# Performance work log

Hardware: AMD Instinct MI355X
Metric: run time of the kernel (lower is better)

The kernel has to match this reference:

```python
import jax, jax.numpy as jnp
import numpy as np

N_NODES = 100000
N_EDGES = 1200000
N_GRAPHS = 1000
HID = 64
OUT = 4
ALPHA_FLAG = 0.03
NEG_SLOPE = 0.2


def _glorot(key, shape):
    fan_in, fan_out = shape[0], shape[-1]
    lim = (6.0 / (fan_in + fan_out)) ** 0.5
    return jax.random.uniform(key, shape, jnp.float32, -lim, lim)


def setup_inputs() -> dict:
    key = jax.random.key(0)
    ks = jax.random.split(key, 32)
    inp = {
        "x": jax.random.normal(ks[0], (N_NODES, 8), jnp.float32),
        "edge_index": jax.random.randint(ks[1], (2, N_EDGES), 0, N_NODES, jnp.int32),
        "batch": jnp.sort(jax.random.randint(ks[2], (N_NODES,), 0, N_GRAPHS, jnp.int32)),
        "climber": jax.random.normal(ks[3], (N_GRAPHS, 6), jnp.float32),
        # lin_in
        "W_in": _glorot(ks[4], (6, HID)), "b_in": jnp.zeros((HID,), jnp.float32),
        # climber_embed: LayerNorm(6) + Linear(6,64)
        "ln_g": jnp.ones((6,), jnp.float32), "ln_b": jnp.zeros((6,), jnp.float32),
        "W_c": _glorot(ks[5], (6, HID)), "b_c": jnp.zeros((HID,), jnp.float32),
        # film1 / film2: Linear(64,128)
        "Wf1": _glorot(ks[6], (HID, 2 * HID)), "bf1": jnp.zeros((2 * HID,), jnp.float32),
        "Wf2": _glorot(ks[7], (HID, 2 * HID)), "bf2": jnp.zeros((2 * HID,), jnp.float32),
        # GATConv 1 (heads=1): lin weight, att_src, att_dst, bias
        "Wg1": _glorot(ks[8], (HID, HID)), "as1": _glorot(ks[9], (HID, 1))[:, 0],
        "ad1": _glorot(ks[10], (HID, 1))[:, 0], "bg1": jnp.zeros((HID,), jnp.float32),
        # GATConv 2
        "Wg2": _glorot(ks[11], (HID, HID)), "as2": _glorot(ks[12], (HID, 1))[:, 0],
        "ad2": _glorot(ks[13], (HID, 1))[:, 0], "bg2": jnp.zeros((HID,), jnp.float32),
        # cls head
        "Wc1": _glorot(ks[14], (HID, HID)), "bc1": jnp.zeros((HID,), jnp.float32),
        "Wc2": _glorot(ks[15], (HID, OUT)), "bc2": jnp.zeros((OUT,), jnp.float32),
        # flag head
        "Wh1": _glorot(ks[16], (2, 8)), "bh1": jnp.zeros((8,), jnp.float32),
        "Wh2": _glorot(ks[17], (8, OUT)), "bh2": jnp.zeros((OUT,), jnp.float32),
    }
    return inp


def _gat(h, src, dst, W, a_src, a_dst, bias, n):
    # PyG GATConv, heads=1, concat=False, self-loops already appended.
    z = h @ W                                    # [N, H]
    e = jax.nn.leaky_relu((z @ a_src)[src] + (z @ a_dst)[dst], NEG_SLOPE)  # [E]
    m = jax.ops.segment_max(e, dst, num_segments=n)
    ex = jnp.exp(e - m[dst])
    s = jax.ops.segment_sum(ex, dst, num_segments=n)
    alpha = ex / (s[dst] + 1e-16)
    out = jax.ops.segment_sum(alpha[:, None] * z[src], dst, num_segments=n)
    return out + bias


def reference(x, edge_index, batch, climber, W_in, b_in, ln_g, ln_b, W_c, b_c,
              Wf1, bf1, Wf2, bf2, Wg1, as1, ad1, bg1, Wg2, as2, ad2, bg2,
              Wc1, bc1, Wc2, bc2, Wh1, bh1, Wh2, bh2):
    n = x.shape[0]
    # add self loops (PyG GATConv default)
    loop = jnp.arange(n, dtype=edge_index.dtype)
    src = jnp.concatenate([edge_index[0], loop])
    dst = jnp.concatenate([edge_index[1], loop])

    x_cont, flags = x[:, :6], x[:, 6:8]
    h = x_cont @ W_in + b_in

    # climber embed: LayerNorm + Linear + ReLU
    mu = jnp.mean(climber, -1, keepdims=True)
    var = jnp.var(climber, -1, keepdims=True)
    cn = (climber - mu) * jax.lax.rsqrt(var + 1e-5) * ln_g + ln_b
    c = jax.nn.relu(cn @ W_c + b_c)

    def film(h, Wf, bf):
        gb = c @ Wf + bf
        gamma, beta = jnp.split(gb, 2, axis=-1)
        return h * (1.0 + gamma[batch]) + beta[batch]

    h = film(h, Wf1, bf1)
    h = jax.nn.relu(_gat(h, src, dst, Wg1, as1, ad1, bg1, n))
    h = film(h, Wf2, bf2)
    h = jax.nn.relu(_gat(h, src, dst, Wg2, as2, ad2, bg2, n))

    # cls head (dropout inactive in eval)
    cls = jax.nn.relu(h @ Wc1 + bc1) @ Wc2 + bc2
    flag = jax.nn.relu(flags @ Wh1 + bh1) @ Wh2 + bh2
    return cls + ALPHA_FLAG * flag
```

## Files before the change

### kernel.cpp

```cpp
#include <hip/hip_runtime.h>
#include <math.h>

#define N_NODES 100000
#define N_EDGES 1200000
#define N_GRAPHS 1000
#define HID 64
#define NBUCK 256
#define NPB   391
#define BCAP  8192
#define EDGE_CHUNK 16384
#define S3_BLOCKS ((N_EDGES + EDGE_CHUNK - 1) / EDGE_CHUNK)
#define LOG2E 1.4426950408889634f
#define N_TILES (N_NODES / 16)
#define MFMA_BLOCKS 391

typedef _Float16 half_t;
typedef __attribute__((ext_vector_type(4))) _Float16 half4;
typedef __attribute__((ext_vector_type(8))) _Float16 half8;
typedef __attribute__((ext_vector_type(4))) float floatx4;

__global__ void k_climber_film(const float* __restrict__ climber,
                               const float* __restrict__ ln_g, const float* __restrict__ ln_b,
                               const float* __restrict__ W_c, const float* __restrict__ b_c,
                               const float* __restrict__ Wf1, const float* __restrict__ bf1,
                               const float* __restrict__ Wf2, const float* __restrict__ bf2,
                               float* __restrict__ gb1, float* __restrict__ gb2,
                               int* __restrict__ bucket_fill) {
    __shared__ float cl[64];
    int g = blockIdx.x;
    int j = threadIdx.x;
    if (g == 0) {
        bucket_fill[j] = 0;
        bucket_fill[j + 128] = 0;
    }
    if (j < 64) {
        float v[6];
        float mu = 0.f;
        #pragma unroll
        for (int k = 0; k < 6; k++) { v[k] = climber[g*6+k]; mu += v[k]; }
        mu *= (1.f/6.f);
        float var = 0.f;
        #pragma unroll
        for (int k = 0; k < 6; k++) { float d = v[k]-mu; var += d*d; }
        var *= (1.f/6.f);
        float rs = rsqrtf(var + 1e-5f);
        float acc = b_c[j];
        #pragma unroll
        for (int k = 0; k < 6; k++) {
            float cn = (v[k]-mu)*rs*ln_g[k] + ln_b[k];
            acc += cn * W_c[k*64+j];
        }
        cl[j] = fmaxf(acc, 0.f);
    }
    __syncthreads();
    float a1 = bf1[j], a2 = bf2[j];
    #pragma unroll 8
    for (int k = 0; k < 64; k++) {
        float ck = cl[k];
        a1 += ck * Wf1[k*128+j];
        a2 += ck * Wf2[k*128+j];
    }
    gb1[g*128+j] = a1;
    gb2[g*128+j] = a2;
}


__global__ void k_bin(const int* __restrict__ ei, int* __restrict__ bucket_fill,
                      int* __restrict__ staged) {
    __shared__ int hist[NBUCK];
    __shared__ int cursor[NBUCK];
    for (int t = threadIdx.x; t < NBUCK; t += blockDim.x) hist[t] = 0;
    __syncthreads();
    int e0 = blockIdx.x * EDGE_CHUNK;
    int e1 = min(e0 + EDGE_CHUNK, N_EDGES);
    for (int e = e0 + threadIdx.x; e < e1; e += blockDim.x)
        atomicAdd(&hist[ei[N_EDGES + e] / NPB], 1);
    __syncthreads();
    if (threadIdx.x < NBUCK) {
        int hv = hist[threadIdx.x];
        int start = threadIdx.x * BCAP;
        if (hv) start += atomicAdd(&bucket_fill[threadIdx.x], hv);
        cursor[threadIdx.x] = start;
    }
    __syncthreads();
    for (int e = e0 + threadIdx.x; e < e1; e += blockDim.x) {
        int src = ei[e], dst = ei[N_EDGES + e];
        int b = dst / NPB;
        int ldst = dst - b * NPB;
        int pos = atomicAdd(&cursor[b], 1);
        staged[pos] = (ldst << 17) | src;
    }
}

__global__ void k_bcsr(const int* __restrict__ staged, const int* __restrict__ bucket_fill,
                       int* __restrict__ rowptr, int* __restrict__ csr_src) {
    __shared__ int bb[NBUCK];
    __shared__ int ldeg[NPB];
    __shared__ int sc[512];
    __shared__ int cursor[NPB];
    int b = blockIdx.x;
    if (threadIdx.x < NBUCK) bb[threadIdx.x] = bucket_fill[threadIdx.x];
    __syncthreads();
    for (int off = 1; off < NBUCK; off <<= 1) {
        int u = 0;
        if (threadIdx.x < NBUCK && threadIdx.x >= off) u = bb[threadIdx.x - off];
        __syncthreads();
        if (threadIdx.x < NBUCK) bb[threadIdx.x] += u;
        __syncthreads();
    }
    int bbase = (b == 0) ? 0 : bb[b-1];
    int bcnt  = bb[b] - bbase;
    const int* st = staged + b * BCAP;
    int n0 = b * NPB;
    int n1 = min(n0 + NPB, N_NODES);
    int nn = n1 - n0;
    for (int t = threadIdx.x; t < NPB; t += blockDim.x) ldeg[t] = 0;
    __syncthreads();
    for (int k = threadIdx.x; k < bcnt; k += blockDim.x)
        atomicAdd(&ldeg[st[k] >> 17], 1);
    __syncthreads();
    if (threadIdx.x < 512) sc[threadIdx.x] = (threadIdx.x < nn) ? ldeg[threadIdx.x] : 0;
    __syncthreads();
    for (int off = 1; off < 512; off <<= 1) {
        int u = 0;
        if (threadIdx.x < 512 && threadIdx.x >= off) u = sc[threadIdx.x - off];
        __syncthreads();
        if (threadIdx.x < 512) sc[threadIdx.x] += u;
        __syncthreads();
    }
    if (threadIdx.x < nn) {
        int pre = sc[threadIdx.x] - ldeg[threadIdx.x];
        rowptr[n0 + threadIdx.x] = bbase + pre;
        cursor[threadIdx.x] = bbase + pre;
    }
    if (b == 0 && threadIdx.x == 0) rowptr[N_NODES] = bb[NBUCK-1];
    __syncthreads();
    for (int k = threadIdx.x; k < bcnt; k += blockDim.x) {
        int v = st[k];
        int pos = atomicAdd(&cursor[v >> 17], 1);
        csr_src[pos] = v & 0x1FFFF;
    }
}

__global__ __launch_bounds__(256) void k_mfma_z1(
        const float* __restrict__ x, const int* __restrict__ batch,
        const float* __restrict__ W_in, const float* __restrict__ b_in,
        const float* __restrict__ gb1, const float* __restrict__ W,
        const float* __restrict__ a_src, const float* __restrict__ a_dst,
        half_t* __restrict__ z, float* __restrict__ es, float* __restrict__ ed) {
    __shared__ float Wi[384];
    __shared__ float bi[64];
    __shared__ half_t zl[4][16*64];
    for (int idx = threadIdx.x; idx < 384; idx += 256) Wi[idx] = W_in[idx];
    if (threadIdx.x < 64) bi[threadIdx.x] = b_in[threadIdx.x];
    int wave = threadIdx.x >> 6;
    int l    = threadIdx.x & 63;
    int c    = l & 15;
    int g    = l >> 4;
    half8 Bf[2][4];
    #pragma unroll
    for (int ko = 0; ko < 2; ko++) {
        #pragma unroll
        for (int nt = 0; nt < 4; nt++) {
            half8 bvec;
            #pragma unroll
            for (int j = 0; j < 8; j++)
                bvec[j] = (half_t)W[(ko*32 + g*8 + j)*64 + c + 16*nt];
            Bf[ko][nt] = bvec;
        }
    }
    float as4[4], ad4[4];
    #pragma unroll
    for (int nt = 0; nt < 4; nt++) {
        as4[nt] = a_src[c + 16*nt] * LOG2E;
        ad4[nt] = a_dst[c + 16*nt] * LOG2E;
    }
    __syncthreads();
    int nWaves = gridDim.x * 4;
    int wid = blockIdx.x * 4 + wave;
    half_t* zw = zl[wave];
    for (int t = wid; t < N_TILES; t += nWaves) {
        int m0 = t * 16;
        int i = m0 + c;
        float xv[6];
        #pragma unroll
        for (int kk = 0; kk < 6; kk++) xv[kk] = x[i*8 + kk];
        int bg_ = batch[i];
        half8 A[2];
        #pragma unroll
        for (int s = 0; s < 2; s++) {
            int bk = s*32 + g*8;
            float acc[8];
            #pragma unroll
            for (int j = 0; j < 8; j++) acc[j] = bi[bk + j];
            #pragma unroll
            for (int kk = 0; kk < 6; kk++) {
                float xk = xv[kk];
                float4 w0 = *(const float4*)&Wi[kk*64 + bk];
                float4 w1 = *(const float4*)&Wi[kk*64 + bk + 4];
                acc[0] += xk*w0.x; acc[1] += xk*w0.y;
                acc[2] += xk*w0.z; acc[3] += xk*w0.w;
                acc[4] += xk*w1.x; acc[5] += xk*w1.y;
                acc[6] += xk*w1.z; acc[7] += xk*w1.w;
            }
            const float4* gbv = (const float4*)(gb1 + bg_*128);
            float4 ga0 = gbv[bk/4],      ga1 = gbv[bk/4 + 1];
            float4 be0 = gbv[16 + bk/4], be1 = gbv[16 + bk/4 + 1];
            half8 hv;
            hv[0] = (half_t)(acc[0]*(1.f+ga0.x) + be0.x);
            hv[1] = (half_t)(acc[1]*(1.f+ga0.y) + be0.y);
            hv[2] = (half_t)(acc[2]*(1.f+ga0.z) + be0.z);
            hv[3] = (half_t)(acc[3]*(1.f+ga0.w) + be0.w);
            hv[4] = (half_t)(acc[4]*(1.f+ga1.x) + be1.x);
            hv[5] = (half_t)(acc[5]*(1.f+ga1.y) + be1.y);
            hv[6] = (half_t)(acc[6]*(1.f+ga1.z) + be1.z);
            hv[7] = (half_t)(acc[7]*(1.f+ga1.w) + be1.w);
            A[s] = hv;
        }
        floatx4 D[4];
        #pragma unroll
        for (int nt = 0; nt < 4; nt++) {
            floatx4 acc = {0.f, 0.f, 0.f, 0.f};
            acc = __builtin_amdgcn_mfma_f32_16x16x32_f16(A[0], Bf[0][nt], acc, 0, 0, 0);
            acc = __builtin_amdgcn_mfma_f32_16x16x32_f16(A[1], Bf[1][nt], acc, 0, 0, 0);
            D[nt] = acc;
        }
        #pragma unroll
        for (int r = 0; r < 4; r++) {
            float ps = D[0][r]*as4[0] + D[1][r]*as4[1] + D[2][r]*as4[2] + D[3][r]*as4[3];
            float pd = D[0][r]*ad4[0] + D[1][r]*ad4[1] + D[2][r]*ad4[2] + D[3][r]*ad4[3];
            #pragma unroll
            for (int off = 1; off < 16; off <<= 1) {
                ps += __shfl_xor(ps, off, 16);
                pd += __shfl_xor(pd, off, 16);
            }
            if (c == 0) {
                es[m0 + g*4 + r] = ps;
                ed[m0 + g*4 + r] = pd;
            }
        }
        #pragma unroll
        for (int nt = 0; nt < 4; nt++) {
            #pragma unroll
            for (int r = 0; r < 4; r++)
                zw[(g*4 + r)*64 + c + 16*nt] = (half_t)D[nt][r];
        }
        __asm__ __volatile__("s_waitcnt lgkmcnt(0)" ::: "memory");
        const half8* zr = (const half8*)zw;
        half8 v0 = zr[l*2];
        half8 v1 = zr[l*2 + 1];
        half8* zo = (half8*)(z + (size_t)m0 * 64);
        zo[l*2]     = v0;
        zo[l*2 + 1] = v1;
        __asm__ __volatile__("s_waitcnt lgkmcnt(0)" ::: "memory");
    }
}

__global__ __launch_bounds__(256) void k_mfma_z(
        const half_t* __restrict__ h, const float* __restrict__ W,
        const float* __restrict__ a_src, const float* __restrict__ a_dst,
        half_t* __restrict__ z, float* __restrict__ es, float* __restrict__ ed) {
    __shared__ half_t zl[4][16*64];
    int wave = threadIdx.x >> 6;
    int l    = threadIdx.x & 63;
    int c    = l & 15;
    int g    = l >> 4;
    half8 Bf[2][4];
    #pragma unroll
    for (int ko = 0; ko < 2; ko++) {
        #pragma unroll
        for (int nt = 0; nt < 4; nt++) {
            half8 b;
            #pragma unroll
            for (int j = 0; j < 8; j++)
                b[j] = (half_t)W[(ko*32 + g*8 + j)*64 + c + 16*nt];
            Bf[ko][nt] = b;
        }
    }
    float as4[4], ad4[4];
    #pragma unroll
    for (int nt = 0; nt < 4; nt++) {
        as4[nt] = a_src[c + 16*nt] * LOG2E;
        ad4[nt] = a_dst[c + 16*nt] * LOG2E;
    }
    int nWaves = gridDim.x * 4;
    int wid = blockIdx.x * 4 + wave;
    half_t* zw = zl[wave];
    for (int t = wid; t < N_TILES; t += nWaves) {
        int m0 = t * 16;
        const half8* hrow = (const half8*)(h + (size_t)(m0 + c) * 64);
        half8 A0 = hrow[g];
        half8 A1 = hrow[g + 4];
        floatx4 D[4];
        #pragma unroll
        for (int nt = 0; nt < 4; nt++) {
            floatx4 acc = {0.f, 0.f, 0.f, 0.f};
            acc = __builtin_amdgcn_mfma_f32_16x16x32_f16(A0, Bf[0][nt], acc, 0, 0, 0);
            acc = __builtin_amdgcn_mfma_f32_16x16x32_f16(A1, Bf[1][nt], acc, 0, 0, 0);
            D[nt] = acc;
        }
        #pragma unroll
        for (int r = 0; r < 4; r++) {
            float ps = D[0][r]*as4[0] + D[1][r]*as4[1] + D[2][r]*as4[2] + D[3][r]*as4[3];
            float pd = D[0][r]*ad4[0] + D[1][r]*ad4[1] + D[2][r]*ad4[2] + D[3][r]*ad4[3];
            #pragma unroll
            for (int off = 1; off < 16; off <<= 1) {
                ps += __shfl_xor(ps, off, 16);
                pd += __shfl_xor(pd, off, 16);
            }
            if (c == 0) {
                es[m0 + g*4 + r] = ps;
                ed[m0 + g*4 + r] = pd;
            }
        }
        #pragma unroll
        for (int nt = 0; nt < 4; nt++) {
            #pragma unroll
            for (int r = 0; r < 4; r++)
                zw[(g*4 + r)*64 + c + 16*nt] = (half_t)D[nt][r];
        }
        __asm__ __volatile__("s_waitcnt lgkmcnt(0)" ::: "memory");
        const half8* zr = (const half8*)zw;
        half8 v0 = zr[l*2];
        half8 v1 = zr[l*2 + 1];
        half8* zo = (half8*)(z + (size_t)m0 * 64);
        zo[l*2]     = v0;
        zo[l*2 + 1] = v1;
        __asm__ __volatile__("s_waitcnt lgkmcnt(0)" ::: "memory");
    }
}

__device__ __forceinline__ float4 h4_to_f4(half4 h) {
    float4 f;
    f.x = (float)h.x; f.y = (float)h.y; f.z = (float)h.z; f.w = (float)h.w;
    return f;
}

__global__ void k_agg(const int* __restrict__ rowptr, const int* __restrict__ csr_src,
                      const float* __restrict__ es, const float* __restrict__ ed,
                      const half_t* __restrict__ z, const float* __restrict__ bg,
                      const int* __restrict__ batch, const float* __restrict__ gb,
                      int apply_film, half_t* __restrict__ hout) {
    int tid = blockIdx.x * blockDim.x + threadIdx.x;
    int i  = tid >> 4;
    int sl = threadIdx.x & 15;
    if (i >= N_NODES) return;
    int beg = rowptr[i], end = rowptr[i+1];
    int deg = end - beg;
    float edi = ed[i];

    float e_self = es[i] + edi;
    e_self = fmaxf(e_self, 0.2f * e_self);

    int svA = 0, svB = 0;
    float exA = 0.f, exB = 0.f;
    if (sl < deg) {
        svA = csr_src[beg + sl];
        float v = es[svA] + edi;
        exA = exp2f(fmaxf(v, 0.2f * v));
    }
    if (16 + sl < deg) {
        svB = csr_src[beg + 16 + sl];
        float v = es[svB] + edi;
        exB = exp2f(fmaxf(v, 0.2f * v));
    }
    float s = exA + exB;
    #pragma unroll
    for (int off = 1; off < 16; off <<= 1)
        s += __shfl_xor(s, off, 16);
    float ex = exp2f(e_self);
    s += ex;

    const half4* z4 = (const half4*)z;
    float4 zi = h4_to_f4(z4[i*16 + sl]);
    float4 acc = {ex*zi.x, ex*zi.y, ex*zi.z, ex*zi.w};

    int lim = (deg < 32) ? deg : 32;
    int k = 0;
    for (; k + 8 <= lim; k += 8) {
        int a[8]; float e[8];
        if (k < 16) {
            #pragma unroll
            for (int j = 0; j < 8; j++) {
                a[j] = __shfl(svA, k+j, 16);
                e[j] = __shfl(exA, k+j, 16);
            }
        } else {
            #pragma unroll
            for (int j = 0; j < 8; j++) {
                a[j] = __shfl(svB, k-16+j, 16);
                e[j] = __shfl(exB, k-16+j, 16);
            }
        }
        half4 q[8];
        #pragma unroll
        for (int j = 0; j < 8; j++) q[j] = z4[a[j]*16 + sl];
        #pragma unroll
        for (int j = 0; j < 8; j++) {
            float4 r = h4_to_f4(q[j]);
            acc.x += e[j]*r.x; acc.y += e[j]*r.y;
            acc.z += e[j]*r.z; acc.w += e[j]*r.w;
        }
    }
    for (; k + 4 <= lim; k += 4) {
        int a[4]; float e[4];
        if (k < 16) {
            #pragma unroll
            for (int j = 0; j < 4; j++) {
                a[j] = __shfl(svA, k+j, 16);
                e[j] = __shfl(exA, k+j, 16);
            }
        } else {
            #pragma unroll
            for (int j = 0; j < 4; j++) {
                a[j] = __shfl(svB, k-16+j, 16);
                e[j] = __shfl(exB, k-16+j, 16);
            }
        }
        half4 q[4];
        #pragma unroll
        for (int j = 0; j < 4; j++) q[j] = z4[a[j]*16 + sl];
        #pragma unroll
        for (int j = 0; j < 4; j++) {
            float4 r = h4_to_f4(q[j]);
            acc.x += e[j]*r.x; acc.y += e[j]*r.y;
            acc.z += e[j]*r.z; acc.w += e[j]*r.w;
        }
    }
    for (; k < lim; k++) {
        int a; float e2;
        if (k < 16) { a = __shfl(svA, k, 16);    e2 = __shfl(exA, k, 16); }
        else        { a = __shfl(svB, k-16, 16); e2 = __shfl(exB, k-16, 16); }
        float4 zr = h4_to_f4(z4[a*16 + sl]);
        acc.x += e2*zr.x; acc.y += e2*zr.y; acc.z += e2*zr.z; acc.w += e2*zr.w;
    }
    for (int kk = beg + 32; kk < end; kk++) {
        int sv = csr_src[kk];
        float v = es[sv] + edi;
        float e2 = exp2f(fmaxf(v, 0.2f * v));
        s += e2;
        float4 zr = h4_to_f4(z4[sv*16 + sl]);
        acc.x += e2*zr.x; acc.y += e2*zr.y; acc.z += e2*zr.z; acc.w += e2*zr.w;
    }
    float inv = 1.f / (s + 1e-16f);
    float4 bg4 = ((const float4*)bg)[sl];
    float4 o;
    o.x = fmaxf(acc.x*inv + bg4.x, 0.f);
    o.y = fmaxf(acc.y*inv + bg4.y, 0.f);
    o.z = fmaxf(acc.z*inv + bg4.z, 0.f);
    o.w = fmaxf(acc.w*inv + bg4.w, 0.f);
    if (apply_film) {
        int g = batch[i];
        const float4* gb4 = (const float4*)gb;
        float4 ga = gb4[g*32 + sl];
        float4 be = gb4[g*32 + 16 + sl];
        o.x = o.x*(1.f+ga.x) + be.x;
        o.y = o.y*(1.f+ga.y) + be.y;
        o.z = o.z*(1.f+ga.z) + be.z;
        o.w = o.w*(1.f+ga.w) + be.w;
    }
    half4 hv;
    hv.x = (half_t)o.x; hv.y = (half_t)o.y; hv.z = (half_t)o.z; hv.w = (half_t)o.w;
    ((half4*)hout)[i*16 + sl] = hv;
}

__global__ __launch_bounds__(256) void k_head_mfma(
        const half_t* __restrict__ h, const float* __restrict__ x,
        const float* __restrict__ Wc1, const float* __restrict__ bc1,
        const float* __restrict__ Wc2, const float* __restrict__ bc2,
        const float* __restrict__ Wh1, const float* __restrict__ bh1,
        const float* __restrict__ Wh2, const float* __restrict__ bh2,
        float* __restrict__ out) {
    int l    = threadIdx.x & 63;
    int c    = l & 15;
    int g    = l >> 4;
    half8 Bf[2][4];
    #pragma unroll
    for (int ko = 0; ko < 2; ko++) {
        #pragma unroll
        for (int nt = 0; nt < 4; nt++) {
            half8 b;
            #pragma unroll
            for (int j = 0; j < 8; j++)
                b[j] = (half_t)Wc1[(ko*32 + g*8 + j)*64 + c + 16*nt];
            Bf[ko][nt] = b;
        }
    }
    float bc1v[4];
    float4 w2[4];
    #pragma unroll
    for (int nt = 0; nt < 4; nt++) {
        bc1v[nt] = bc1[c + 16*nt];
        w2[nt] = ((const float4*)Wc2)[c + 16*nt];
    }
    int nWaves = gridDim.x * 4;
    int wid = blockIdx.x * 4 + (threadIdx.x >> 6);
    for (int t = wid; t < N_TILES; t += nWaves) {
        int m0 = t * 16;
        const half8* hrow = (const half8*)(h + (size_t)(m0 + c) * 64);
        half8 A0 = hrow[g];
        half8 A1 = hrow[g + 4];
        floatx4 D[4];
        #pragma unroll
        for (int nt = 0; nt < 4; nt++) {
            floatx4 acc = {0.f, 0.f, 0.f, 0.f};
            acc = __builtin_amdgcn_mfma_f32_16x16x32_f16(A0, Bf[0][nt], acc, 0, 0, 0);
            acc = __builtin_amdgcn_mfma_f32_16x16x32_f16(A1, Bf[1][nt], acc, 0, 0, 0);
            D[nt] = acc;
        }
        #pragma unroll
        for (int r = 0; r < 4; r++) {
            float4 p = {0.f, 0.f, 0.f, 0.f};
            #pragma unroll
            for (int nt = 0; nt < 4; nt++) {
                float tv = fmaxf(D[nt][r] + bc1v[nt], 0.f);
                p.x += tv * w2[nt].x;
                p.y += tv * w2[nt].y;
                p.z += tv * w2[nt].z;
                p.w += tv * w2[nt].w;
            }
            #pragma unroll
            for (int off = 1; off < 16; off <<= 1) {
                p.x += __shfl_xor(p.x, off, 16);
                p.y += __shfl_xor(p.y, off, 16);
                p.z += __shfl_xor(p.z, off, 16);
                p.w += __shfl_xor(p.w, off, 16);
            }
            if (c == 0) {
                int m = m0 + g*4 + r;
                float f0 = x[m*8+6], f1 = x[m*8+7];
                float t8[8];
                #pragma unroll
                for (int q = 0; q < 8; q++)
                    t8[q] = fmaxf(f0*Wh1[q] + f1*Wh1[8+q] + bh1[q], 0.f);
                float fl[4];
                #pragma unroll
                for (int q = 0; q < 4; q++) {
                    float a = bh2[q];
                    #pragma unroll
                    for (int rr = 0; rr < 8; rr++) a += t8[rr]*Wh2[rr*4+q];
                    fl[q] = a;
                }
                float4 ov;
                ov.x = p.x + bc2[0] + 0.03f*fl[0];
                ov.y = p.y + bc2[1] + 0.03f*fl[1];
                ov.z = p.z + bc2[2] + 0.03f*fl[2];
                ov.w = p.w + bc2[3] + 0.03f*fl[3];
                ((float4*)out)[m] = ov;
            }
        }
    }
}

extern "C" void kernel_launch(void* const* d_in, const int* in_sizes, int n_in,
                              void* d_out, int out_size, void* d_ws, size_t ws_size,
                              hipStream_t stream) {
    const float* x       = (const float*)d_in[0];
    const int*   ei      = (const int*)  d_in[1];
    const int*   batch   = (const int*)  d_in[2];
    const float* climber = (const float*)d_in[3];
    const float* W_in    = (const float*)d_in[4];
    const float* b_in    = (const float*)d_in[5];
    const float* ln_g    = (const float*)d_in[6];
    const float* ln_b    = (const float*)d_in[7];
    const float* W_c     = (const float*)d_in[8];
    const float* b_c     = (const float*)d_in[9];
    const float* Wf1     = (const float*)d_in[10];
    const float* bf1     = (const float*)d_in[11];
    const float* Wf2     = (const float*)d_in[12];
    const float* bf2     = (const float*)d_in[13];
    const float* Wg1     = (const float*)d_in[14];
    const float* as1     = (const float*)d_in[15];
    const float* ad1     = (const float*)d_in[16];
    const float* bg1     = (const float*)d_in[17];
    const float* Wg2     = (const float*)d_in[18];
    const float* as2     = (const float*)d_in[19];
    const float* ad2     = (const float*)d_in[20];
    const float* bg2     = (const float*)d_in[21];
    const float* Wc1     = (const float*)d_in[22];
    const float* bc1     = (const float*)d_in[23];
    const float* Wc2     = (const float*)d_in[24];
    const float* bc2     = (const float*)d_in[25];
    const float* Wh1     = (const float*)d_in[26];
    const float* bh1     = (const float*)d_in[27];
    const float* Wh2     = (const float*)d_in[28];
    const float* bh2     = (const float*)d_in[29];
    float* out = (float*)d_out;
    float* ws  = (float*)d_ws;

    float*  gb1         = ws;
    float*  gb2         = gb1 + 128000;
    half_t* hbuf        = (half_t*)(gb2 + 128000);
    half_t* zbuf        = hbuf + 6400000;
    float*  es          = (float*)(zbuf + 6400000);
    float*  ed          = es + N_NODES;
    int*    rowptr      = (int*)(ed + N_NODES);
    int*    csr_src     = rowptr + N_NODES + 1;
    int*    bucket_fill = csr_src + N_EDGES;
    int*    staged      = bucket_fill + NBUCK;

    k_climber_film<<<N_GRAPHS, 128, 0, stream>>>(climber, ln_g, ln_b, W_c, b_c,
                                                 Wf1, bf1, Wf2, bf2, gb1, gb2,
                                                 bucket_fill);

    k_bin <<<S3_BLOCKS, 1024, 0, stream>>>(ei, bucket_fill, staged);
    k_bcsr<<<NBUCK, 1024, 0, stream>>>(staged, bucket_fill, rowptr, csr_src);

    int nodeBlocks = (N_NODES*16 + 255)/256;
    k_mfma_z1<<<MFMA_BLOCKS, 256, 0, stream>>>(x, batch, W_in, b_in, gb1, Wg1,
                                               as1, ad1, zbuf, es, ed);
    k_agg<<<nodeBlocks, 256, 0, stream>>>(rowptr, csr_src, es, ed, zbuf, bg1,
                                          batch, gb2, 1, hbuf);
    k_mfma_z<<<MFMA_BLOCKS, 256, 0, stream>>>(hbuf, Wg2, as2, ad2, zbuf, es, ed);
    k_agg<<<nodeBlocks, 256, 0, stream>>>(rowptr, csr_src, es, ed, zbuf, bg2,
                                          batch, gb2, 0, hbuf);
    k_head_mfma<<<MFMA_BLOCKS, 256, 0, stream>>>(hbuf, x, Wc1, bc1, Wc2, bc2,
                                                 Wh1, bh1, Wh2, bh2, out);
}
```

Measured before the change: 259.3 us.

## Merge setup kernels, slice feature layout by channel group, and pre-pack weights

Merges the climber/FiLM, weight pre-packing and edge binning into one launch, and runs CSR build alongside the first z projection in another. Node features are stored as 8 channel slices of 8 halves, and aggregation gives each block a single slice, so the gathered rows per pass fit better in cache. Edge chunks are smaller to spread binning over more blocks, and MFMA weights are packed once instead of being converted per block. The cost is more aggregation blocks, each redoing the softmax weight computation for every slice, plus larger fused kernels that may limit occupancy.

```diff
diff --git a/kernel.cpp b/kernel.cpp
--- a/kernel.cpp
+++ b/kernel.cpp
@@ -8,70 +8,92 @@
 #define NBUCK 256
 #define NPB   391
 #define BCAP  8192
-#define EDGE_CHUNK 16384
+#define EDGE_CHUNK 4096
 #define S3_BLOCKS ((N_EDGES + EDGE_CHUNK - 1) / EDGE_CHUNK)
+#define PRE_FILM_BLOCKS 125
+#define PRE_BIN0 127
+#define Z1_BLOCKS 256
 #define LOG2E 1.4426950408889634f
 #define N_TILES (N_NODES / 16)
+#define SLICE 800000
+#define NSL 8
+#define AGG_CHUNKS ((N_NODES + 63) / 64)
+#define AGGS_BLOCKS (NSL * AGG_CHUNKS)
 #define MFMA_BLOCKS 391
 
 typedef _Float16 half_t;
+typedef __attribute__((ext_vector_type(2))) _Float16 half2v;
 typedef __attribute__((ext_vector_type(4))) _Float16 half4;
 typedef __attribute__((ext_vector_type(8))) _Float16 half8;
 typedef __attribute__((ext_vector_type(4))) float floatx4;
 
-__global__ void k_climber_film(const float* __restrict__ climber,
-                               const float* __restrict__ ln_g, const float* __restrict__ ln_b,
-                               const float* __restrict__ W_c, const float* __restrict__ b_c,
-                               const float* __restrict__ Wf1, const float* __restrict__ bf1,
-                               const float* __restrict__ Wf2, const float* __restrict__ bf2,
-                               float* __restrict__ gb1, float* __restrict__ gb2,
-                               int* __restrict__ bucket_fill) {
-    __shared__ float cl[64];
-    int g = blockIdx.x;
-    int j = threadIdx.x;
-    if (g == 0) {
-        bucket_fill[j] = 0;
-        bucket_fill[j + 128] = 0;
-    }
-    if (j < 64) {
-        float v[6];
-        float mu = 0.f;
-        #pragma unroll
-        for (int k = 0; k < 6; k++) { v[k] = climber[g*6+k]; mu += v[k]; }
-        mu *= (1.f/6.f);
-        float var = 0.f;
-        #pragma unroll
-        for (int k = 0; k < 6; k++) { float d = v[k]-mu; var += d*d; }
-        var *= (1.f/6.f);
-        float rs = rsqrtf(var + 1e-5f);
-        float acc = b_c[j];
-        #pragma unroll
-        for (int k = 0; k < 6; k++) {
-            float cn = (v[k]-mu)*rs*ln_g[k] + ln_b[k];
-            acc += cn * W_c[k*64+j];
-        }
-        cl[j] = fmaxf(acc, 0.f);
-    }
-    __syncthreads();
-    float a1 = bf1[j], a2 = bf2[j];
-    #pragma unroll 8
-    for (int k = 0; k < 64; k++) {
-        float ck = cl[k];
-        a1 += ck * Wf1[k*128+j];
-        a2 += ck * Wf2[k*128+j];
-    }
-    gb1[g*128+j] = a1;
-    gb2[g*128+j] = a2;
-}
-
-
-__global__ void k_bin(const int* __restrict__ ei, int* __restrict__ bucket_fill,
-                      int* __restrict__ staged) {
+__global__ __launch_bounds__(1024) void k_pre(
+        const float* __restrict__ climber,
+        const float* __restrict__ ln_g, const float* __restrict__ ln_b,
+        const float* __restrict__ W_c, const float* __restrict__ b_c,
+        const float* __restrict__ Wf1, const float* __restrict__ bf1,
+        const float* __restrict__ Wf2, const float* __restrict__ bf2,
+        const float* __restrict__ Wg2, const float* __restrict__ Wc1,
+        float* __restrict__ gb1, float* __restrict__ gb2,
+        half_t* __restrict__ Wp1, half_t* __restrict__ Wp2,
+        const int* __restrict__ ei, int* __restrict__ bucket_fill,
+        int* __restrict__ staged) {
+    int bid = blockIdx.x;
+    if (bid < PRE_FILM_BLOCKS) {
+        __shared__ float cl[8][64];
+        int sub = threadIdx.x >> 7;
+        int j   = threadIdx.x & 127;
+        int g   = bid * 8 + sub;
+        if (j < 64) {
+            float v[6];
+            float mu = 0.f;
+            #pragma unroll
+            for (int k = 0; k < 6; k++) { v[k] = climber[g*6+k]; mu += v[k]; }
+            mu *= (1.f/6.f);
+            float var = 0.f;
+            #pragma unroll
+            for (int k = 0; k < 6; k++) { float d = v[k]-mu; var += d*d; }
+            var *= (1.f/6.f);
+            float rs = rsqrtf(var + 1e-5f);
+            float acc = b_c[j];
+            #pragma unroll
+            for (int k = 0; k < 6; k++) {
+                float cn = (v[k]-mu)*rs*ln_g[k] + ln_b[k];
+                acc += cn * W_c[k*64+j];
+            }
+            cl[sub][j] = fmaxf(acc, 0.f);
+        }
+        __syncthreads();
+        float a1 = bf1[j], a2 = bf2[j];
+        #pragma unroll 8
+        for (int k = 0; k < 64; k++) {
+            float ck = cl[sub][k];
+            a1 += ck * Wf1[k*128+j];
+            a2 += ck * Wf2[k*128+j];
+        }
+        gb1[g*128+j] = a1;
+        gb2[g*128+j] = a2;
+        return;
+    }
+    if (bid < PRE_BIN0) {
+        const float* Wsrc = (bid == PRE_FILM_BLOCKS) ? Wg2 : Wc1;
+        half_t*      Wdst = (bid == PRE_FILM_BLOCKS) ? Wp1 : Wp2;
+        for (int idx = threadIdx.x; idx < 4096; idx += 1024) {
+            int jj = idx & 7;
+            int ko = (idx >> 3) & 1;
+            int l  = (idx >> 4) & 63;
+            int w  = idx >> 10;
+            int c  = l & 15;
+            int gg = l >> 4;
+            Wdst[idx] = (half_t)Wsrc[(ko*32 + gg*8 + jj)*64 + c + 16*w];
+        }
+        return;
+    }
     __shared__ int hist[NBUCK];
     __shared__ int cursor[NBUCK];
     for (int t = threadIdx.x; t < NBUCK; t += blockDim.x) hist[t] = 0;
     __syncthreads();
-    int e0 = blockIdx.x * EDGE_CHUNK;
+    int e0 = (bid - PRE_BIN0) * EDGE_CHUNK;
     int e1 = min(e0 + EDGE_CHUNK, N_EDGES);
     for (int e = e0 + threadIdx.x; e < e1; e += blockDim.x)
         atomicAdd(&hist[ei[N_EDGES + e] / NPB], 1);
@@ -92,66 +114,67 @@
     }
 }
 
-__global__ void k_bcsr(const int* __restrict__ staged, const int* __restrict__ bucket_fill,
-                       int* __restrict__ rowptr, int* __restrict__ csr_src) {
-    __shared__ int bb[NBUCK];
-    __shared__ int ldeg[NPB];
-    __shared__ int sc[512];
-    __shared__ int cursor[NPB];
-    int b = blockIdx.x;
-    if (threadIdx.x < NBUCK) bb[threadIdx.x] = bucket_fill[threadIdx.x];
-    __syncthreads();
-    for (int off = 1; off < NBUCK; off <<= 1) {
-        int u = 0;
-        if (threadIdx.x < NBUCK && threadIdx.x >= off) u = bb[threadIdx.x - off];
-        __syncthreads();
-        if (threadIdx.x < NBUCK) bb[threadIdx.x] += u;
-        __syncthreads();
-    }
-    int bbase = (b == 0) ? 0 : bb[b-1];
-    int bcnt  = bb[b] - bbase;
-    const int* st = staged + b * BCAP;
-    int n0 = b * NPB;
-    int n1 = min(n0 + NPB, N_NODES);
-    int nn = n1 - n0;
-    for (int t = threadIdx.x; t < NPB; t += blockDim.x) ldeg[t] = 0;
-    __syncthreads();
-    for (int k = threadIdx.x; k < bcnt; k += blockDim.x)
-        atomicAdd(&ldeg[st[k] >> 17], 1);
-    __syncthreads();
-    if (threadIdx.x < 512) sc[threadIdx.x] = (threadIdx.x < nn) ? ldeg[threadIdx.x] : 0;
-    __syncthreads();
-    for (int off = 1; off < 512; off <<= 1) {
-        int u = 0;
-        if (threadIdx.x < 512 && threadIdx.x >= off) u = sc[threadIdx.x - off];
-        __syncthreads();
-        if (threadIdx.x < 512) sc[threadIdx.x] += u;
-        __syncthreads();
-    }
-    if (threadIdx.x < nn) {
-        int pre = sc[threadIdx.x] - ldeg[threadIdx.x];
-        rowptr[n0 + threadIdx.x] = bbase + pre;
-        cursor[threadIdx.x] = bbase + pre;
-    }
-    if (b == 0 && threadIdx.x == 0) rowptr[N_NODES] = bb[NBUCK-1];
-    __syncthreads();
-    for (int k = threadIdx.x; k < bcnt; k += blockDim.x) {
-        int v = st[k];
-        int pos = atomicAdd(&cursor[v >> 17], 1);
-        csr_src[pos] = v & 0x1FFFF;
-    }
-}
-
-__global__ __launch_bounds__(256) void k_mfma_z1(
+__global__ __launch_bounds__(1024) void k_mid(
+        const int* __restrict__ staged, const int* __restrict__ bucket_fill,
+        int* __restrict__ rowptr, int* __restrict__ csr_src,
         const float* __restrict__ x, const int* __restrict__ batch,
         const float* __restrict__ W_in, const float* __restrict__ b_in,
         const float* __restrict__ gb1, const float* __restrict__ W,
         const float* __restrict__ a_src, const float* __restrict__ a_dst,
         half_t* __restrict__ z, float* __restrict__ es, float* __restrict__ ed) {
+    if (blockIdx.x < NBUCK) {
+        __shared__ int bb[NBUCK];
+        __shared__ int ldeg[NPB];
+        __shared__ int sc[512];
+        __shared__ int cursor[NPB];
+        int b = blockIdx.x;
+        if (threadIdx.x < NBUCK) bb[threadIdx.x] = bucket_fill[threadIdx.x];
+        __syncthreads();
+        for (int off = 1; off < NBUCK; off <<= 1) {
+            int u = 0;
+            if (threadIdx.x < NBUCK && threadIdx.x >= off) u = bb[threadIdx.x - off];
+            __syncthreads();
+            if (threadIdx.x < NBUCK) bb[threadIdx.x] += u;
+            __syncthreads();
+        }
+        int bbase = (b == 0) ? 0 : bb[b-1];
+        int bcnt  = bb[b] - bbase;
+        const int* st = staged + b * BCAP;
+        int n0 = b * NPB;
+        int n1 = min(n0 + NPB, N_NODES);
+        int nn = n1 - n0;
+        for (int t = threadIdx.x; t < NPB; t += blockDim.x) ldeg[t] = 0;
+        __syncthreads();
+        for (int k = threadIdx.x; k < bcnt; k += blockDim.x)
+            atomicAdd(&ldeg[st[k] >> 17], 1);
+        __syncthreads();
+        if (threadIdx.x < 512) sc[threadIdx.x] = (threadIdx.x < nn) ? ldeg[threadIdx.x] : 0;
+        __syncthreads();
+        for (int off = 1; off < 512; off <<= 1) {
+            int u = 0;
+            if (threadIdx.x < 512 && threadIdx.x >= off) u = sc[threadIdx.x - off];
+            __syncthreads();
+            if (threadIdx.x < 512) sc[threadIdx.x] += u;
+            __syncthreads();
+        }
+        if (threadIdx.x < nn) {
+            int pre = sc[threadIdx.x] - ldeg[threadIdx.x];
+            rowptr[n0 + threadIdx.x] = bbase + pre;
+            cursor[threadIdx.x] = bbase + pre;
+        }
+        if (b == 0 && threadIdx.x == 0) rowptr[N_NODES] = bb[NBUCK-1];
+        __syncthreads();
+        for (int k = threadIdx.x; k < bcnt; k += blockDim.x) {
+            int v = st[k];
+            int pos = atomicAdd(&cursor[v >> 17], 1);
+            csr_src[pos] = v & 0x1FFFF;
+        }
+        return;
+    }
     __shared__ float Wi[384];
     __shared__ float bi[64];
-    __shared__ half_t zl[4][16*64];
-    for (int idx = threadIdx.x; idx < 384; idx += 256) Wi[idx] = W_in[idx];
+    __shared__ __align__(16) half_t zl[16][1024];
+    for (int idx = threadIdx.x; idx < 384; idx += 1024) Wi[idx] = W_in[idx];
     if (threadIdx.x < 64) bi[threadIdx.x] = b_in[threadIdx.x];
     int wave = threadIdx.x >> 6;
     int l    = threadIdx.x & 63;
@@ -176,15 +199,16 @@
         ad4[nt] = a_dst[c + 16*nt] * LOG2E;
     }
     __syncthreads();
-    int nWaves = gridDim.x * 4;
-    int wid = blockIdx.x * 4 + wave;
+    int nWaves = Z1_BLOCKS * 16;
+    int wid = (blockIdx.x - NBUCK) * 16 + wave;
     half_t* zw = zl[wave];
+    const float4* x4p = (const float4*)x;
     for (int t = wid; t < N_TILES; t += nWaves) {
         int m0 = t * 16;
         int i = m0 + c;
-        float xv[6];
-        #pragma unroll
-        for (int kk = 0; kk < 6; kk++) xv[kk] = x[i*8 + kk];
+        float4 xa = x4p[i*2];
+        float4 xb = x4p[i*2 + 1];
+        float xv[6] = {xa.x, xa.y, xa.z, xa.w, xb.x, xb.y};
         int bg_ = batch[i];
         half8 A[2];
         #pragma unroll
@@ -246,37 +270,165 @@
                 zw[(g*4 + r)*64 + c + 16*nt] = (half_t)D[nt][r];
         }
         __asm__ __volatile__("s_waitcnt lgkmcnt(0)" ::: "memory");
-        const half8* zr = (const half8*)zw;
-        half8 v0 = zr[l*2];
-        half8 v1 = zr[l*2 + 1];
-        half8* zo = (half8*)(z + (size_t)m0 * 64);
-        zo[l*2]     = v0;
-        zo[l*2 + 1] = v1;
+        int sI = l >> 4, nI = l & 15;
+        *(half8*)(z + (size_t)sI*SLICE     + (size_t)(m0+nI)*8) = *(const half8*)&zw[nI*64 + sI*8];
+        *(half8*)(z + (size_t)(sI+4)*SLICE + (size_t)(m0+nI)*8) = *(const half8*)&zw[nI*64 + (sI+4)*8];
         __asm__ __volatile__("s_waitcnt lgkmcnt(0)" ::: "memory");
     }
 }
 
-__global__ __launch_bounds__(256) void k_mfma_z(
-        const half_t* __restrict__ h, const float* __restrict__ W,
+__global__ __launch_bounds__(256) void k_aggS(
+        const int* __restrict__ rowptr, const int* __restrict__ csr_src,
+        const float* __restrict__ es, const float* __restrict__ ed,
+        const half_t* __restrict__ zS, const float* __restrict__ bgv,
+        const int* __restrict__ batch, const float* __restrict__ gb,
+        int apply_film, half_t* __restrict__ hS) {
+    int slice = blockIdx.x & 7;
+    int chunk = blockIdx.x >> 3;
+    int grp = threadIdx.x >> 2;
+    int q   = threadIdx.x & 3;
+    int i = chunk * 64 + grp;
+    bool valid = (i < N_NODES);
+    int ii = valid ? i : 0;
+    const half_t* zs = zS + (size_t)slice * SLICE;
+
+    int beg = rowptr[ii], end = rowptr[ii+1];
+    int deg = valid ? (end - beg) : 0;
+    float edi = ed[ii];
+
+    int idA[4];
+    #pragma unroll
+    for (int j = 0; j < 4; j++) {
+        int k = j*4 + q;
+        idA[j] = (k < deg) ? csr_src[beg + k] : 0;
+    }
+    bool big = (deg > 16);
+    int idB[4] = {0,0,0,0};
+    if (big) {
+        #pragma unroll
+        for (int j = 0; j < 4; j++) {
+            int k = 16 + j*4 + q;
+            idB[j] = (k < deg) ? csr_src[beg + k] : 0;
+        }
+    }
+
+    int sv16[16];
+    #pragma unroll
+    for (int j = 0; j < 4; j++)
+        #pragma unroll
+        for (int qq = 0; qq < 4; qq++)
+            sv16[j*4+qq] = __shfl(idA[j], qq, 4);
+    half2v qv[16];
+    #pragma unroll
+    for (int k = 0; k < 16; k++)
+        qv[k] = *(const half2v*)(zs + (size_t)sv16[k]*8 + q*2);
+    half2v zself = *(const half2v*)(zs + (size_t)ii*8 + q*2);
+
+    float exA[4];
+    #pragma unroll
+    for (int j = 0; j < 4; j++) {
+        float v = es[idA[j]] + edi;
+        v = fmaxf(v, 0.2f * v);
+        exA[j] = (j*4 + q < deg) ? exp2f(v) : 0.f;
+    }
+    float exB[4] = {0.f, 0.f, 0.f, 0.f};
+    if (big) {
+        #pragma unroll
+        for (int j = 0; j < 4; j++) {
+            float v = es[idB[j]] + edi;
+            v = fmaxf(v, 0.2f * v);
+            exB[j] = (16 + j*4 + q < deg) ? exp2f(v) : 0.f;
+        }
+    }
+    float s = exA[0]+exA[1]+exA[2]+exA[3] + exB[0]+exB[1]+exB[2]+exB[3];
+    s += __shfl_xor(s, 1, 4);
+    s += __shfl_xor(s, 2, 4);
+    float vs = es[ii] + edi;
+    vs = fmaxf(vs, 0.2f * vs);
+    float e_self = exp2f(vs);
+    s += e_self;
+
+    float ax = e_self * (float)zself[0];
+    float ay = e_self * (float)zself[1];
+
+    if (deg > 32) {
+        for (int kk = beg + 32; kk < end; kk++) {
+            int sv = csr_src[kk];
+            float v = es[sv] + edi;
+            float e2 = exp2f(fmaxf(v, 0.2f * v));
+            s += e2;
+            half2v zr = *(const half2v*)(zs + (size_t)sv*8 + q*2);
+            ax += e2 * (float)zr[0];
+            ay += e2 * (float)zr[1];
+        }
+    }
+
+    #pragma unroll
+    for (int j = 0; j < 4; j++) {
+        #pragma unroll
+        for (int qq = 0; qq < 4; qq++) {
+            float e = __shfl(exA[j], qq, 4);
+            half2v r = qv[j*4+qq];
+            ax += e * (float)r[0];
+            ay += e * (float)r[1];
+        }
+    }
+    if (big) {
+        int sv2[16];
+        #pragma unroll
+        for (int j = 0; j < 4; j++)
+            #pragma unroll
+            for (int qq = 0; qq < 4; qq++)
+                sv2[j*4+qq] = __shfl(idB[j], qq, 4);
+        half2v qv2[16];
+        #pragma unroll
+        for (int k = 0; k < 16; k++)
+            qv2[k] = *(const half2v*)(zs + (size_t)sv2[k]*8 + q*2);
+        #pragma unroll
+        for (int j = 0; j < 4; j++) {
+            #pragma unroll
+            for (int qq = 0; qq < 4; qq++) {
+                float e = __shfl(exB[j], qq, 4);
+                half2v r = qv2[j*4+qq];
+                ax += e * (float)r[0];
+                ay += e * (float)r[1];
+            }
+        }
+    }
+
+    float inv = 1.f / (s + 1e-16f);
+    float2 bgl = *(const float2*)(bgv + slice*8 + q*2);
+    float ox = fmaxf(ax*inv + bgl.x, 0.f);
+    float oy = fmaxf(ay*inv + bgl.y, 0.f);
+    if (apply_film) {
+        int g = batch[ii];
+        float2 ga = *(const float2*)(gb + g*128 + slice*8 + q*2);
+        float2 be = *(const float2*)(gb + g*128 + 64 + slice*8 + q*2);
+        ox = ox*(1.f+ga.x) + be.x;
+        oy = oy*(1.f+ga.y) + be.y;
+    }
+    if (valid) {
+        half2v hv;
+        hv[0] = (half_t)ox; hv[1] = (half_t)oy;
+        *(half2v*)(hS + (size_t)slice*SLICE + (size_t)i*8 + q*2) = hv;
+    }
+}
+
+__global__ __launch_bounds__(256) void k_zt(
+        const half_t* __restrict__ hS, const half_t* __restrict__ Wp,
         const float* __restrict__ a_src, const float* __restrict__ a_dst,
-        half_t* __restrict__ z, float* __restrict__ es, float* __restrict__ ed) {
-    __shared__ half_t zl[4][16*64];
+        half_t* __restrict__ zSo, float* __restrict__ es_o, float* __restrict__ ed_o) {
+    __shared__ __align__(16) half_t zl[4][1024];
     int wave = threadIdx.x >> 6;
     int l    = threadIdx.x & 63;
     int c    = l & 15;
     int g    = l >> 4;
     half8 Bf[2][4];
     #pragma unroll
-    for (int ko = 0; ko < 2; ko++) {
-        #pragma unroll
-        for (int nt = 0; nt < 4; nt++) {
-            half8 b;
-            #pragma unroll
-            for (int j = 0; j < 8; j++)
-                b[j] = (half_t)W[(ko*32 + g*8 + j)*64 + c + 16*nt];
-            Bf[ko][nt] = b;
-        }
-    }
+    for (int nt = 0; nt < 4; nt++)
+        #pragma unroll
+        for (int ko = 0; ko < 2; ko++)
+            Bf[ko][nt] = *(const half8*)(Wp + (((size_t)nt*64 + l)*2 + ko)*8);
     float as4[4], ad4[4];
     #pragma unroll
     for (int nt = 0; nt < 4; nt++) {
@@ -288,9 +440,8 @@
     half_t* zw = zl[wave];
     for (int t = wid; t < N_TILES; t += nWaves) {
         int m0 = t * 16;
-        const half8* hrow = (const half8*)(h + (size_t)(m0 + c) * 64);
-        half8 A0 = hrow[g];
-        half8 A1 = hrow[g + 4];
+        half8 A0 = *(const half8*)(hS + (size_t)g*SLICE     + (size_t)(m0+c)*8);
+        half8 A1 = *(const half8*)(hS + (size_t)(g+4)*SLICE + (size_t)(m0+c)*8);
         floatx4 D[4];
         #pragma unroll
         for (int nt = 0; nt < 4; nt++) {
@@ -309,8 +460,8 @@
                 pd += __shfl_xor(pd, off, 16);
             }
             if (c == 0) {
-                es[m0 + g*4 + r] = ps;
-                ed[m0 + g*4 + r] = pd;
+                es_o[m0 + g*4 + r] = ps;
+                ed_o[m0 + g*4 + r] = pd;
             }
         }
         #pragma unroll
@@ -320,154 +471,18 @@
                 zw[(g*4 + r)*64 + c + 16*nt] = (half_t)D[nt][r];
         }
         __asm__ __volatile__("s_waitcnt lgkmcnt(0)" ::: "memory");
-        const half8* zr = (const half8*)zw;
-        half8 v0 = zr[l*2];
-        half8 v1 = zr[l*2 + 1];
-        half8* zo = (half8*)(z + (size_t)m0 * 64);
-        zo[l*2]     = v0;
-        zo[l*2 + 1] = v1;
+        int sI = l >> 4, nI = l & 15;
+        *(half8*)(zSo + (size_t)sI*SLICE     + (size_t)(m0+nI)*8) = *(const half8*)&zw[nI*64 + sI*8];
+        *(half8*)(zSo + (size_t)(sI+4)*SLICE + (size_t)(m0+nI)*8) = *(const half8*)&zw[nI*64 + (sI+4)*8];
         __asm__ __volatile__("s_waitcnt lgkmcnt(0)" ::: "memory");
     }
 }
 
-__device__ __forceinline__ float4 h4_to_f4(half4 h) {
-    float4 f;
-    f.x = (float)h.x; f.y = (float)h.y; f.z = (float)h.z; f.w = (float)h.w;
-    return f;
-}
-
-__global__ void k_agg(const int* __restrict__ rowptr, const int* __restrict__ csr_src,
-                      const float* __restrict__ es, const float* __restrict__ ed,
-                      const half_t* __restrict__ z, const float* __restrict__ bg,
-                      const int* __restrict__ batch, const float* __restrict__ gb,
-                      int apply_film, half_t* __restrict__ hout) {
-    int tid = blockIdx.x * blockDim.x + threadIdx.x;
-    int i  = tid >> 4;
-    int sl = threadIdx.x & 15;
-    if (i >= N_NODES) return;
-    int beg = rowptr[i], end = rowptr[i+1];
-    int deg = end - beg;
-    float edi = ed[i];
-
-    float e_self = es[i] + edi;
-    e_self = fmaxf(e_self, 0.2f * e_self);
-
-    int svA = 0, svB = 0;
-    float exA = 0.f, exB = 0.f;
-    if (sl < deg) {
-        svA = csr_src[beg + sl];
-        float v = es[svA] + edi;
-        exA = exp2f(fmaxf(v, 0.2f * v));
-    }
-    if (16 + sl < deg) {
-        svB = csr_src[beg + 16 + sl];
-        float v = es[svB] + edi;
-        exB = exp2f(fmaxf(v, 0.2f * v));
-    }
-    float s = exA + exB;
-    #pragma unroll
-    for (int off = 1; off < 16; off <<= 1)
-        s += __shfl_xor(s, off, 16);
-    float ex = exp2f(e_self);
-    s += ex;
-
-    const half4* z4 = (const half4*)z;
-    float4 zi = h4_to_f4(z4[i*16 + sl]);
-    float4 acc = {ex*zi.x, ex*zi.y, ex*zi.z, ex*zi.w};
-
-    int lim = (deg < 32) ? deg : 32;
-    int k = 0;
-    for (; k + 8 <= lim; k += 8) {
-        int a[8]; float e[8];
-        if (k < 16) {
-            #pragma unroll
-            for (int j = 0; j < 8; j++) {
-                a[j] = __shfl(svA, k+j, 16);
-                e[j] = __shfl(exA, k+j, 16);
-            }
-        } else {
-            #pragma unroll
-            for (int j = 0; j < 8; j++) {
-                a[j] = __shfl(svB, k-16+j, 16);
-                e[j] = __shfl(exB, k-16+j, 16);
-            }
-        }
-        half4 q[8];
-        #pragma unroll
-        for (int j = 0; j < 8; j++) q[j] = z4[a[j]*16 + sl];
-        #pragma unroll
-        for (int j = 0; j < 8; j++) {
-            float4 r = h4_to_f4(q[j]);
-            acc.x += e[j]*r.x; acc.y += e[j]*r.y;
-            acc.z += e[j]*r.z; acc.w += e[j]*r.w;
-        }
-    }
-    for (; k + 4 <= lim; k += 4) {
-        int a[4]; float e[4];
-        if (k < 16) {
-            #pragma unroll
-            for (int j = 0; j < 4; j++) {
-                a[j] = __shfl(svA, k+j, 16);
-                e[j] = __shfl(exA, k+j, 16);
-            }
-        } else {
-            #pragma unroll
-            for (int j = 0; j < 4; j++) {
-                a[j] = __shfl(svB, k-16+j, 16);
-                e[j] = __shfl(exB, k-16+j, 16);
-            }
-        }
-        half4 q[4];
-        #pragma unroll
-        for (int j = 0; j < 4; j++) q[j] = z4[a[j]*16 + sl];
-        #pragma unroll
-        for (int j = 0; j < 4; j++) {
-            float4 r = h4_to_f4(q[j]);
-            acc.x += e[j]*r.x; acc.y += e[j]*r.y;
-            acc.z += e[j]*r.z; acc.w += e[j]*r.w;
-        }
-    }
-    for (; k < lim; k++) {
-        int a; float e2;
-        if (k < 16) { a = __shfl(svA, k, 16);    e2 = __shfl(exA, k, 16); }
-        else        { a = __shfl(svB, k-16, 16); e2 = __shfl(exB, k-16, 16); }
-        float4 zr = h4_to_f4(z4[a*16 + sl]);
-        acc.x += e2*zr.x; acc.y += e2*zr.y; acc.z += e2*zr.z; acc.w += e2*zr.w;
-    }
-    for (int kk = beg + 32; kk < end; kk++) {
-        int sv = csr_src[kk];
-        float v = es[sv] + edi;
-        float e2 = exp2f(fmaxf(v, 0.2f * v));
-        s += e2;
-        float4 zr = h4_to_f4(z4[sv*16 + sl]);
-        acc.x += e2*zr.x; acc.y += e2*zr.y; acc.z += e2*zr.z; acc.w += e2*zr.w;
-    }
-    float inv = 1.f / (s + 1e-16f);
-    float4 bg4 = ((const float4*)bg)[sl];
-    float4 o;
-    o.x = fmaxf(acc.x*inv + bg4.x, 0.f);
-    o.y = fmaxf(acc.y*inv + bg4.y, 0.f);
-    o.z = fmaxf(acc.z*inv + bg4.z, 0.f);
-    o.w = fmaxf(acc.w*inv + bg4.w, 0.f);
-    if (apply_film) {
-        int g = batch[i];
-        const float4* gb4 = (const float4*)gb;
-        float4 ga = gb4[g*32 + sl];
-        float4 be = gb4[g*32 + 16 + sl];
-        o.x = o.x*(1.f+ga.x) + be.x;
-        o.y = o.y*(1.f+ga.y) + be.y;
-        o.z = o.z*(1.f+ga.z) + be.z;
-        o.w = o.w*(1.f+ga.w) + be.w;
-    }
-    half4 hv;
-    hv.x = (half_t)o.x; hv.y = (half_t)o.y; hv.z = (half_t)o.z; hv.w = (half_t)o.w;
-    ((half4*)hout)[i*16 + sl] = hv;
-}
-
-__global__ __launch_bounds__(256) void k_head_mfma(
-        const half_t* __restrict__ h, const float* __restrict__ x,
-        const float* __restrict__ Wc1, const float* __restrict__ bc1,
-        const float* __restrict__ Wc2, const float* __restrict__ bc2,
+__global__ __launch_bounds__(256) void k_head(
+        const half_t* __restrict__ hS, const float* __restrict__ x,
+        const half_t* __restrict__ Wp,
+        const float* __restrict__ bc1, const float* __restrict__ Wc2,
+        const float* __restrict__ bc2,
         const float* __restrict__ Wh1, const float* __restrict__ bh1,
         const float* __restrict__ Wh2, const float* __restrict__ bh2,
         float* __restrict__ out) {
@@ -476,16 +491,10 @@
     int g    = l >> 4;
     half8 Bf[2][4];
     #pragma unroll
-    for (int ko = 0; ko < 2; ko++) {
-        #pragma unroll
-        for (int nt = 0; nt < 4; nt++) {
-            half8 b;
-            #pragma unroll
-            for (int j = 0; j < 8; j++)
-                b[j] = (half_t)Wc1[(ko*32 + g*8 + j)*64 + c + 16*nt];
-            Bf[ko][nt] = b;
-        }
-    }
+    for (int nt = 0; nt < 4; nt++)
+        #pragma unroll
+        for (int ko = 0; ko < 2; ko++)
+            Bf[ko][nt] = *(const half8*)(Wp + (((size_t)nt*64 + l)*2 + ko)*8);
     float bc1v[4];
     float4 w2[4];
     #pragma unroll
@@ -497,9 +506,8 @@
     int wid = blockIdx.x * 4 + (threadIdx.x >> 6);
     for (int t = wid; t < N_TILES; t += nWaves) {
         int m0 = t * 16;
-        const half8* hrow = (const half8*)(h + (size_t)(m0 + c) * 64);
-        half8 A0 = hrow[g];
-        half8 A1 = hrow[g + 4];
+        half8 A0 = *(const half8*)(hS + (size_t)g*SLICE     + (size_t)(m0+c)*8);
+        half8 A1 = *(const half8*)(hS + (size_t)(g+4)*SLICE + (size_t)(m0+c)*8);
         floatx4 D[4];
         #pragma unroll
         for (int nt = 0; nt < 4; nt++) {
@@ -531,15 +539,15 @@
                 float f0 = x[m*8+6], f1 = x[m*8+7];
                 float t8[8];
                 #pragma unroll
-                for (int q = 0; q < 8; q++)
-                    t8[q] = fmaxf(f0*Wh1[q] + f1*Wh1[8+q] + bh1[q], 0.f);
+                for (int qq = 0; qq < 8; qq++)
+                    t8[qq] = fmaxf(f0*Wh1[qq] + f1*Wh1[8+qq] + bh1[qq], 0.f);
                 float fl[4];
                 #pragma unroll
-                for (int q = 0; q < 4; q++) {
-                    float a = bh2[q];
+                for (int qq = 0; qq < 4; qq++) {
+                    float a = bh2[qq];
                     #pragma unroll
-                    for (int rr = 0; rr < 8; rr++) a += t8[rr]*Wh2[rr*4+q];
-                    fl[q] = a;
+                    for (int rr = 0; rr < 8; rr++) a += t8[rr]*Wh2[rr*4+qq];
+                    fl[qq] = a;
                 }
                 float4 ov;
                 ov.x = p.x + bc2[0] + 0.03f*fl[0];
@@ -590,30 +598,40 @@
 
     float*  gb1         = ws;
     float*  gb2         = gb1 + 128000;
-    half_t* hbuf        = (half_t*)(gb2 + 128000);
-    half_t* zbuf        = hbuf + 6400000;
-    float*  es          = (float*)(zbuf + 6400000);
-    float*  ed          = es + N_NODES;
-    int*    rowptr      = (int*)(ed + N_NODES);
+    half_t* Wp1         = (half_t*)(gb2 + 128000);
+    half_t* Wp2         = Wp1 + 4096;
+    half_t* zS_A        = Wp2 + 4096;
+    half_t* hS1         = zS_A + NSL*SLICE;
+    half_t* zS_B        = hS1 + NSL*SLICE;
+    half_t* hS2         = zS_B + NSL*SLICE;
+    float*  es1         = (float*)(hS2 + NSL*SLICE);
+    float*  ed1         = es1 + N_NODES;
+    float*  es2         = ed1 + N_NODES;
+    float*  ed2         = es2 + N_NODES;
+    int*    rowptr      = (int*)(ed2 + N_NODES);
     int*    csr_src     = rowptr + N_NODES + 1;
     int*    bucket_fill = csr_src + N_EDGES;
     int*    staged      = bucket_fill + NBUCK;
 
-    k_climber_film<<<N_GRAPHS, 128, 0, stream>>>(climber, ln_g, ln_b, W_c, b_c,
-                                                 Wf1, bf1, Wf2, bf2, gb1, gb2,
-                                                 bucket_fill);
-
-    k_bin <<<S3_BLOCKS, 1024, 0, stream>>>(ei, bucket_fill, staged);
-    k_bcsr<<<NBUCK, 1024, 0, stream>>>(staged, bucket_fill, rowptr, csr_src);
-
-    int nodeBlocks = (N_NODES*16 + 255)/256;
-    k_mfma_z1<<<MFMA_BLOCKS, 256, 0, stream>>>(x, batch, W_in, b_in, gb1, Wg1,
-                                               as1, ad1, zbuf, es, ed);
-    k_agg<<<nodeBlocks, 256, 0, stream>>>(rowptr, csr_src, es, ed, zbuf, bg1,
-                                          batch, gb2, 1, hbuf);
-    k_mfma_z<<<MFMA_BLOCKS, 256, 0, stream>>>(hbuf, Wg2, as2, ad2, zbuf, es, ed);
-    k_agg<<<nodeBlocks, 256, 0, stream>>>(rowptr, csr_src, es, ed, zbuf, bg2,
-                                          batch, gb2, 0, hbuf);
-    k_head_mfma<<<MFMA_BLOCKS, 256, 0, stream>>>(hbuf, x, Wc1, bc1, Wc2, bc2,
-                                                 Wh1, bh1, Wh2, bh2, out);
+    hipMemsetAsync(bucket_fill, 0, NBUCK * sizeof(int), stream);
+
+    k_pre<<<PRE_BIN0 + S3_BLOCKS, 1024, 0, stream>>>(climber, ln_g, ln_b, W_c, b_c,
+                                                     Wf1, bf1, Wf2, bf2, Wg2, Wc1,
+                                                     gb1, gb2, Wp1, Wp2,
+                                                     ei, bucket_fill, staged);
+
+    k_mid<<<NBUCK + Z1_BLOCKS, 1024, 0, stream>>>(staged, bucket_fill, rowptr, csr_src,
+                                                  x, batch, W_in, b_in, gb1, Wg1,
+                                                  as1, ad1, zS_A, es1, ed1);
+
+    k_aggS<<<AGGS_BLOCKS, 256, 0, stream>>>(rowptr, csr_src, es1, ed1, zS_A, bg1,
+                                            batch, gb2, 1, hS1);
+
+    k_zt<<<MFMA_BLOCKS, 256, 0, stream>>>(hS1, Wp1, as2, ad2, zS_B, es2, ed2);
+
+    k_aggS<<<AGGS_BLOCKS, 256, 0, stream>>>(rowptr, csr_src, es2, ed2, zS_B, bg2,
+                                            batch, nullptr, 0, hS2);
+
+    k_head<<<MFMA_BLOCKS, 256, 0, stream>>>(hS2, x, Wp2, bc1, Wc2, bc2,
+                                            Wh1, bh1, Wh2, bh2, out);
 }
```

Measured after the change: 355.6 us. 37.1% more time.
